# Kernel tuning notes

Hardware: AMD Instinct MI355X
Metric: run time of the kernel (lower is better)

## Reference

```python
import jax, jax.numpy as jnp
import numpy as np

T, B, IN, OUT, N_MOD, K = 1024, 8, 1024, 1024, 16, 2

def setup_inputs() -> dict:
    key = jax.random.key(0)
    k1, k2, k3, k4 = jax.random.split(key, 4)
    x = jax.random.normal(k1, (T, B, IN), dtype=jnp.float32)
    selection = jax.random.randint(k2, (B, K), 0, N_MOD, dtype=jnp.int64)
    weight = jax.random.normal(k3, (N_MOD, IN, OUT), dtype=jnp.float32) * (1.0 / np.sqrt(IN))
    bias = jax.random.normal(k4, (N_MOD, OUT), dtype=jnp.float32) * 0.02
    return {"x": x, "selection": selection, "weight": weight, "bias": bias}

def reference(x, selection, weight, bias):
    # time_major=True: x is [T, B, in] -> batch-major [B, T, in]
    xb = jnp.swapaxes(x, 0, 1)
    # Gather the K selected expert weight matrices per batch row: [B, K, in, out]
    W_sel = weight[selection]
    # Equivalent to matmul(x[i], cat(weight[sel], dim=1)): [B, T, K, out]
    o = jnp.einsum('bti,bkio->btko', xb, W_sel)
    Bn, Tn, Kn, On = o.shape
    o = o.reshape(Bn, Tn, Kn * On)
    # concat_dim == 1 bias: bias[sel].view(1, -1) -> [1, K*out], broadcast over T
    o = o + bias[selection].reshape(Bn, 1, Kn * On)
    # back to time-major [T, B, K*out]
    return jnp.swapaxes(o, 0, 1)
```

## Files before the change

kernel.cpp:

```cpp
#include <hip/hip_runtime.h>

#define T_DIM 1024
#define B_DIM 8
#define IN_DIM 1024
#define OUT_DIM 1024
#define N_MODL 16
#define K_SEL 2

typedef unsigned short ushort_t;
typedef __bf16 bf16x8 __attribute__((ext_vector_type(8)));
typedef float f32x4 __attribute__((ext_vector_type(4)));

__device__ __forceinline__ unsigned int f2bf2(float lo, float hi) {
  union { float f; unsigned int u; } a, b; a.f = lo; b.f = hi;
  unsigned int ra = (a.u + 0x7fffu + ((a.u >> 16) & 1u)) >> 16;
  unsigned int rb = (b.u + 0x7fffu + ((b.u >> 16) & 1u)) >> 16;
  return ra | (rb << 16);
}

__device__ __forceinline__ void async_g2l(const void* g, void* l) {
  __builtin_amdgcn_global_load_lds(
      (const __attribute__((address_space(1))) unsigned int*)g,
      (__attribute__((address_space(3))) unsigned int*)l,
      16, 0, 0);
}

__device__ __forceinline__ int read_sel(const int* __restrict__ s, int g) {
  bool i64 = true;
#pragma unroll
  for (int j = 0; j < 8; ++j) i64 &= (s[2 * j + 1] == 0);
  return i64 ? s[2 * g] : s[g];
}

__global__ __launch_bounds__(256) void convert_kernel(const float* __restrict__ x,
                                                      const float* __restrict__ w,
                                                      const int* __restrict__ selp,
                                                      ushort_t* __restrict__ xb,
                                                      ushort_t* __restrict__ wt) {
  __shared__ ushort_t tb[128 * 128];
  const int bid = blockIdx.x;
  if (bid >= 1024) {
    const int i = (bid - 1024) * 256 + threadIdx.x;
    const float4* s = (const float4*)x;
    float4 a = s[i * 2], b = s[i * 2 + 1];
    uint4 o;
    o.x = f2bf2(a.x, a.y); o.y = f2bf2(a.z, a.w);
    o.z = f2bf2(b.x, b.y); o.w = f2bf2(b.z, b.w);
    ((uint4*)xb)[i] = o;
    return;
  }
  const int m = bid >> 6;
  bool used = false;
#pragma unroll
  for (int g = 0; g < B_DIM * K_SEL; ++g) used |= (read_sel(selp, g) == m);
  if (!used) return;

  const int i0 = ((bid >> 3) & 7) * 128;
  const int o0 = (bid & 7) * 128;
  const float* src = w + ((size_t)(m * IN_DIM + i0)) * OUT_DIM + o0;

  const int o4 = (threadIdx.x & 31) * 4;
  const int ib = threadIdx.x >> 5;
#pragma unroll
  for (int p = 0; p < 16; ++p) {
    const int i = ib + p * 8;
    float4 v = *(const float4*)(src + (size_t)i * OUT_DIM + o4);
    const int osw = o4 ^ (((i >> 3) & 15) << 2);
    uint2 d2; d2.x = f2bf2(v.x, v.y); d2.y = f2bf2(v.z, v.w);
    *(uint2*)(tb + i * 128 + osw) = d2;
  }
  __syncthreads();

  ushort_t* dst = wt + ((size_t)(m * OUT_DIM + o0)) * IN_DIM + i0;
  const int il = (threadIdx.x & 15) * 8;
  const int ob = threadIdx.x >> 4;
  const int q2 = ((il >> 3) & 15) << 2;
#pragma unroll
  for (int p = 0; p < 8; ++p) {
    const int o = ob + p * 16;
    const int osw = o ^ q2;
    uint4 d;
    unsigned int u[8];
#pragma unroll
    for (int j = 0; j < 8; ++j) u[j] = tb[(il + j) * 128 + osw];
    d.x = u[0] | (u[1] << 16); d.y = u[2] | (u[3] << 16);
    d.z = u[4] | (u[5] << 16); d.w = u[6] | (u[7] << 16);
    *(uint4*)(dst + (size_t)o * IN_DIM + il) = d;
  }
}

#define MFMA16 __builtin_amdgcn_mfma_f32_16x16x32_bf16

template<bool LAST>
__device__ __forceinline__ void gstep(
    int t, ushort_t* As,
    const ushort_t* curB0, const ushort_t* curB1,
    ushort_t* nxtB0, ushort_t* nxtB1,
    const ushort_t* Ab, const ushort_t* Bb0, const ushort_t* Bb1,
    int wv, int ardo, int brdo, int cb,
    f32x4 (&acc0)[4][4], f32x4 (&acc1)[4][4]) {
  const int k1 = (t + 1) * 64;
  if (!LAST) {
#pragma unroll
    for (int c = 0; c < 4; ++c) {
      const int j = wv * 4 + c;
      async_g2l(Bb0 + (size_t)8 * j * IN_DIM + k1, nxtB0 + j * 512);
      async_g2l(Bb1 + (size_t)8 * j * IN_DIM + k1, nxtB1 + j * 512);
    }
    __builtin_amdgcn_sched_barrier(0);
  }
  bf16x8 af0[4], af1[4];
  const ushort_t* Ard = As + ardo;
#pragma unroll
  for (int i = 0; i < 4; ++i) {
    af0[i] = *(const bf16x8*)(Ard + i * 1024 + cb);
    af1[i] = *(const bf16x8*)(Ard + i * 1024 + (cb ^ 32));
  }
  if (!LAST) {
    __builtin_amdgcn_sched_barrier(0);
    asm volatile("s_waitcnt lgkmcnt(0)" ::: "memory");
    __builtin_amdgcn_sched_barrier(0);
    __builtin_amdgcn_s_barrier();
    __builtin_amdgcn_sched_barrier(0);
#pragma unroll
    for (int c = 0; c < 4; ++c) {
      const int j = wv * 4 + c;
      async_g2l(Ab + (size_t)8 * j * (B_DIM * IN_DIM) + k1, As + j * 512);
    }
    __builtin_amdgcn_sched_barrier(0);
  }
  const ushort_t* Brd0 = curB0 + brdo;
  const ushort_t* Brd1 = curB1 + brdo;
  bf16x8 b0[4], b1[4];
#pragma unroll
  for (int n = 0; n < 4; ++n) {
    b0[n] = *(const bf16x8*)(Brd0 + n * 1024 + cb);
    b1[n] = *(const bf16x8*)(Brd1 + n * 1024 + cb);
  }
  __builtin_amdgcn_s_setprio(1);
#pragma unroll
  for (int mt = 0; mt < 4; ++mt)
#pragma unroll
    for (int nt = 0; nt < 4; ++nt) {
      acc0[mt][nt] = MFMA16(af0[mt], b0[nt], acc0[mt][nt], 0, 0, 0);
      acc1[mt][nt] = MFMA16(af0[mt], b1[nt], acc1[mt][nt], 0, 0, 0);
    }
  __builtin_amdgcn_s_setprio(0);
#pragma unroll
  for (int n = 0; n < 4; ++n) {
    b0[n] = *(const bf16x8*)(Brd0 + n * 1024 + (cb ^ 32));
    b1[n] = *(const bf16x8*)(Brd1 + n * 1024 + (cb ^ 32));
  }
  __builtin_amdgcn_s_setprio(1);
#pragma unroll
  for (int mt = 0; mt < 4; ++mt)
#pragma unroll
    for (int nt = 0; nt < 4; ++nt) {
      acc0[mt][nt] = MFMA16(af1[mt], b0[nt], acc0[mt][nt], 0, 0, 0);
      acc1[mt][nt] = MFMA16(af1[mt], b1[nt], acc1[mt][nt], 0, 0, 0);
    }
  __builtin_amdgcn_s_setprio(0);
  if (!LAST) {
    __builtin_amdgcn_sched_barrier(0);
    asm volatile("s_waitcnt vmcnt(0)" ::: "memory");
    __builtin_amdgcn_sched_barrier(0);
    __builtin_amdgcn_s_barrier();
    __builtin_amdgcn_sched_barrier(0);
  }
}

__global__ __launch_bounds__(256, 2) void mlgemm_kernel(const ushort_t* __restrict__ xb,
                                                        const ushort_t* __restrict__ wt,
                                                        const int* __restrict__ selp,
                                                        const float* __restrict__ bias,
                                                        float* __restrict__ out) {
  __shared__ __align__(16) ushort_t smem[40960];
  ushort_t* As = smem;
#define BSP(buf, e) (smem + 8192 + ((buf) * 2 + (e)) * 8192)

  const int lin = blockIdx.x;
  const int b = lin & 7;
  const int mtile = (lin >> 3) & 7;
  const int ntile = lin >> 6;
  const int e0 = read_sel(selp, 2 * b);
  const int e1 = read_sel(selp, 2 * b + 1);
  const int m0 = mtile * 128;
  const int n0 = ntile * 128;

  const int tid = threadIdx.x;
  const int lane = tid & 63;
  const int wv = tid >> 6;

  const int srow = lane >> 3;
  const int sx = (((lane & 7) ^ (srow & 7)) << 3);
  const ushort_t* Ab  = xb + (size_t)(m0 + srow) * (B_DIM * IN_DIM) + b * IN_DIM + sx;
  const ushort_t* Bb0 = wt + ((size_t)(e0 * OUT_DIM + n0 + srow)) * IN_DIM + sx;
  const ushort_t* Bb1 = wt + ((size_t)(e1 * OUT_DIM + n0 + srow)) * IN_DIM + sx;

  const int frow = lane & 15;
  const int quad = lane >> 4;
  const int cb = ((quad ^ (frow & 7)) << 3);
  const int wrow = (wv & 1) * 64;
  const int wcol = (wv >> 1) * 64;
  const int ardo = (wrow + frow) * 64;
  const int brdo = (wcol + frow) * 64;

  f32x4 acc0[4][4] = {};
  f32x4 acc1[4][4] = {};

#pragma unroll
  for (int c = 0; c < 4; ++c) {
    const int j = wv * 4 + c;
    async_g2l(Ab  + (size_t)8 * j * (B_DIM * IN_DIM), As + j * 512);
    async_g2l(Bb0 + (size_t)8 * j * IN_DIM, BSP(0, 0) + j * 512);
    async_g2l(Bb1 + (size_t)8 * j * IN_DIM, BSP(0, 1) + j * 512);
  }
  __builtin_amdgcn_sched_barrier(0);
  asm volatile("s_waitcnt vmcnt(0)" ::: "memory");
  __builtin_amdgcn_sched_barrier(0);
  __builtin_amdgcn_s_barrier();
  __builtin_amdgcn_sched_barrier(0);

  for (int t = 0; t < 14; t += 2) {
    gstep<false>(t,     As, BSP(0, 0), BSP(0, 1), BSP(1, 0), BSP(1, 1),
                 Ab, Bb0, Bb1, wv, ardo, brdo, cb, acc0, acc1);
    gstep<false>(t + 1, As, BSP(1, 0), BSP(1, 1), BSP(0, 0), BSP(0, 1),
                 Ab, Bb0, Bb1, wv, ardo, brdo, cb, acc0, acc1);
  }
  gstep<false>(14, As, BSP(0, 0), BSP(0, 1), BSP(1, 0), BSP(1, 1),
               Ab, Bb0, Bb1, wv, ardo, brdo, cb, acc0, acc1);
  gstep<true>(15, As, BSP(1, 0), BSP(1, 1), BSP(0, 0), BSP(0, 1),
              Ab, Bb0, Bb1, wv, ardo, brdo, cb, acc0, acc1);

  __syncthreads();

  float* fb = (float*)smem;
  const float* bp0 = bias + (size_t)e0 * OUT_DIM;
  const float* bp1 = bias + (size_t)e1 * OUT_DIM;
  const int ocol0 = n0 + wcol + frow;
  float bv0[4], bv1[4];
#pragma unroll
  for (int nt = 0; nt < 4; ++nt) {
    bv0[nt] = bp0[ocol0 + nt * 16];
    bv1[nt] = bp1[ocol0 + nt * 16];
  }

#pragma unroll
  for (int r = 0; r < 2; ++r) {
    if ((wv & 1) == r) {
#pragma unroll
      for (int mt = 0; mt < 4; ++mt)
#pragma unroll
        for (int rr = 0; rr < 4; ++rr) {
          const int rowl = mt * 16 + quad * 4 + rr;
#pragma unroll
          for (int nt = 0; nt < 4; ++nt) {
            const int col = wcol + frow + nt * 16;
            fb[rowl * 260 + col]       = acc0[mt][nt][rr] + bv0[nt];
            fb[rowl * 260 + 128 + col] = acc1[mt][nt][rr] + bv1[nt];
          }
        }
    }
    __syncthreads();
    const int rl_base = tid >> 5;
    const int lir = tid & 31;
#pragma unroll
    for (int p = 0; p < 16; ++p) {
      const int e = p >> 3;
      const int rowl = (p & 7) * 8 + rl_base;
      const float* s = fb + rowl * 260 + e * 128 + lir * 4;
      float4 v = *(const float4*)s;
      const int grow = m0 + r * 64 + rowl;
      float* d = out + (size_t)grow * (B_DIM * K_SEL * OUT_DIM)
                     + (size_t)b * (K_SEL * OUT_DIM)
                     + (size_t)e * OUT_DIM + n0 + lir * 4;
      *(float4*)d = v;
    }
    __syncthreads();
  }
#undef BSP
}

extern "C" void kernel_launch(void* const* d_in, const int* in_sizes, int n_in,
                              void* d_out, int out_size, void* d_ws, size_t ws_size,
                              hipStream_t stream) {
  const float* x    = (const float*)d_in[0];
  const int*   sel  = (const int*)d_in[1];
  const float* w    = (const float*)d_in[2];
  const float* bias = (const float*)d_in[3];
  float* out = (float*)d_out;

  ushort_t* xb = (ushort_t*)d_ws;
  ushort_t* wt = (ushort_t*)((char*)d_ws +
                             (size_t)T_DIM * B_DIM * IN_DIM * 2);

  convert_kernel<<<dim3(1024 + T_DIM * B_DIM * IN_DIM / 8 / 256), 256, 0, stream>>>(
      x, w, sel, xb, wt);
  mlgemm_kernel<<<dim3(8 * 8 * B_DIM), 256, 0, stream>>>(xb, wt, sel, bias, out);
}
```

Before: 174.9 us.

## Fuse fp32-to-bf16 conversion of x into GEMM A-tile loading

Removes the separate pass that converts x to bf16 in a workspace. The GEMM now loads fp32 x directly into registers, converts to bf16 and writes the swizzled LDS tile itself. This saves a full write and re-read of the bf16 copy of x. In exchange, x is read in fp32 (twice the bytes) by each of the 8 n-tiles, and A loads become synchronous register loads instead of async LDS loads, which adds VGPR pressure and extra LDS store waits.

```diff
diff --git a/kernel.cpp b/kernel.cpp
--- a/kernel.cpp
+++ b/kernel.cpp
@@ -32,23 +32,11 @@
   return i64 ? s[2 * g] : s[g];
 }
 
-__global__ __launch_bounds__(256) void convert_kernel(const float* __restrict__ x,
-                                                      const float* __restrict__ w,
+__global__ __launch_bounds__(256) void convert_kernel(const float* __restrict__ w,
                                                       const int* __restrict__ selp,
-                                                      ushort_t* __restrict__ xb,
                                                       ushort_t* __restrict__ wt) {
   __shared__ ushort_t tb[128 * 128];
   const int bid = blockIdx.x;
-  if (bid >= 1024) {
-    const int i = (bid - 1024) * 256 + threadIdx.x;
-    const float4* s = (const float4*)x;
-    float4 a = s[i * 2], b = s[i * 2 + 1];
-    uint4 o;
-    o.x = f2bf2(a.x, a.y); o.y = f2bf2(a.z, a.w);
-    o.z = f2bf2(b.x, b.y); o.w = f2bf2(b.z, b.w);
-    ((uint4*)xb)[i] = o;
-    return;
-  }
   const int m = bid >> 6;
   bool used = false;
 #pragma unroll
@@ -96,11 +84,20 @@
     int t, ushort_t* As,
     const ushort_t* curB0, const ushort_t* curB1,
     ushort_t* nxtB0, ushort_t* nxtB1,
-    const ushort_t* Ab, const ushort_t* Bb0, const ushort_t* Bb1,
-    int wv, int ardo, int brdo, int cb,
+    const float* Af, const ushort_t* Bb0, const ushort_t* Bb1,
+    int wv, int ardo, int brdo, int cb, int awo,
     f32x4 (&acc0)[4][4], f32x4 (&acc1)[4][4]) {
   const int k1 = (t + 1) * 64;
+  float4 a4[4][2];
   if (!LAST) {
+#pragma unroll
+    for (int c = 0; c < 4; ++c) {
+      const int j = wv * 4 + c;
+      const float* ap = Af + (size_t)8 * j * (B_DIM * IN_DIM) + k1;
+      a4[c][0] = *(const float4*)(ap);
+      a4[c][1] = *(const float4*)(ap + 4);
+    }
+    __builtin_amdgcn_sched_barrier(0);
 #pragma unroll
     for (int c = 0; c < 4; ++c) {
       const int j = wv * 4 + c;
@@ -124,8 +121,10 @@
     __builtin_amdgcn_sched_barrier(0);
 #pragma unroll
     for (int c = 0; c < 4; ++c) {
-      const int j = wv * 4 + c;
-      async_g2l(Ab + (size_t)8 * j * (B_DIM * IN_DIM) + k1, As + j * 512);
+      uint4 o;
+      o.x = f2bf2(a4[c][0].x, a4[c][0].y); o.y = f2bf2(a4[c][0].z, a4[c][0].w);
+      o.z = f2bf2(a4[c][1].x, a4[c][1].y); o.w = f2bf2(a4[c][1].z, a4[c][1].w);
+      *(uint4*)(As + awo + c * 512) = o;
     }
     __builtin_amdgcn_sched_barrier(0);
   }
@@ -162,14 +161,14 @@
   __builtin_amdgcn_s_setprio(0);
   if (!LAST) {
     __builtin_amdgcn_sched_barrier(0);
-    asm volatile("s_waitcnt vmcnt(0)" ::: "memory");
+    asm volatile("s_waitcnt vmcnt(0) lgkmcnt(0)" ::: "memory");
     __builtin_amdgcn_sched_barrier(0);
     __builtin_amdgcn_s_barrier();
     __builtin_amdgcn_sched_barrier(0);
   }
 }
 
-__global__ __launch_bounds__(256, 2) void mlgemm_kernel(const ushort_t* __restrict__ xb,
+__global__ __launch_bounds__(256, 2) void mlgemm_kernel(const float* __restrict__ x,
                                                         const ushort_t* __restrict__ wt,
                                                         const int* __restrict__ selp,
                                                         const float* __restrict__ bias,
@@ -193,9 +192,10 @@
 
   const int srow = lane >> 3;
   const int sx = (((lane & 7) ^ (srow & 7)) << 3);
-  const ushort_t* Ab  = xb + (size_t)(m0 + srow) * (B_DIM * IN_DIM) + b * IN_DIM + sx;
+  const float*    Af  = x  + ((size_t)(m0 + srow) * B_DIM + b) * IN_DIM + sx;
   const ushort_t* Bb0 = wt + ((size_t)(e0 * OUT_DIM + n0 + srow)) * IN_DIM + sx;
   const ushort_t* Bb1 = wt + ((size_t)(e1 * OUT_DIM + n0 + srow)) * IN_DIM + sx;
+  const int awo = wv * 4 * 512 + lane * 8;
 
   const int frow = lane & 15;
   const int quad = lane >> 4;
@@ -208,29 +208,45 @@
   f32x4 acc0[4][4] = {};
   f32x4 acc1[4][4] = {};
 
-#pragma unroll
-  for (int c = 0; c < 4; ++c) {
-    const int j = wv * 4 + c;
-    async_g2l(Ab  + (size_t)8 * j * (B_DIM * IN_DIM), As + j * 512);
-    async_g2l(Bb0 + (size_t)8 * j * IN_DIM, BSP(0, 0) + j * 512);
-    async_g2l(Bb1 + (size_t)8 * j * IN_DIM, BSP(0, 1) + j * 512);
-  }
-  __builtin_amdgcn_sched_barrier(0);
-  asm volatile("s_waitcnt vmcnt(0)" ::: "memory");
-  __builtin_amdgcn_sched_barrier(0);
-  __builtin_amdgcn_s_barrier();
-  __builtin_amdgcn_sched_barrier(0);
+  {
+    float4 p4[4][2];
+#pragma unroll
+    for (int c = 0; c < 4; ++c) {
+      const int j = wv * 4 + c;
+      const float* ap = Af + (size_t)8 * j * (B_DIM * IN_DIM);
+      p4[c][0] = *(const float4*)(ap);
+      p4[c][1] = *(const float4*)(ap + 4);
+    }
+#pragma unroll
+    for (int c = 0; c < 4; ++c) {
+      const int j = wv * 4 + c;
+      async_g2l(Bb0 + (size_t)8 * j * IN_DIM, BSP(0, 0) + j * 512);
+      async_g2l(Bb1 + (size_t)8 * j * IN_DIM, BSP(0, 1) + j * 512);
+    }
+#pragma unroll
+    for (int c = 0; c < 4; ++c) {
+      uint4 o;
+      o.x = f2bf2(p4[c][0].x, p4[c][0].y); o.y = f2bf2(p4[c][0].z, p4[c][0].w);
+      o.z = f2bf2(p4[c][1].x, p4[c][1].y); o.w = f2bf2(p4[c][1].z, p4[c][1].w);
+      *(uint4*)(As + awo + c * 512) = o;
+    }
+    __builtin_amdgcn_sched_barrier(0);
+    asm volatile("s_waitcnt vmcnt(0) lgkmcnt(0)" ::: "memory");
+    __builtin_amdgcn_sched_barrier(0);
+    __builtin_amdgcn_s_barrier();
+    __builtin_amdgcn_sched_barrier(0);
+  }
 
   for (int t = 0; t < 14; t += 2) {
     gstep<false>(t,     As, BSP(0, 0), BSP(0, 1), BSP(1, 0), BSP(1, 1),
-                 Ab, Bb0, Bb1, wv, ardo, brdo, cb, acc0, acc1);
+                 Af, Bb0, Bb1, wv, ardo, brdo, cb, awo, acc0, acc1);
     gstep<false>(t + 1, As, BSP(1, 0), BSP(1, 1), BSP(0, 0), BSP(0, 1),
-                 Ab, Bb0, Bb1, wv, ardo, brdo, cb, acc0, acc1);
+                 Af, Bb0, Bb1, wv, ardo, brdo, cb, awo, acc0, acc1);
   }
   gstep<false>(14, As, BSP(0, 0), BSP(0, 1), BSP(1, 0), BSP(1, 1),
-               Ab, Bb0, Bb1, wv, ardo, brdo, cb, acc0, acc1);
+               Af, Bb0, Bb1, wv, ardo, brdo, cb, awo, acc0, acc1);
   gstep<true>(15, As, BSP(1, 0), BSP(1, 1), BSP(0, 0), BSP(0, 1),
-              Ab, Bb0, Bb1, wv, ardo, brdo, cb, acc0, acc1);
+              Af, Bb0, Bb1, wv, ardo, brdo, cb, awo, acc0, acc1);
 
   __syncthreads();
 
@@ -290,11 +306,8 @@
   const float* bias = (const float*)d_in[3];
   float* out = (float*)d_out;
 
-  ushort_t* xb = (ushort_t*)d_ws;
-  ushort_t* wt = (ushort_t*)((char*)d_ws +
-                             (size_t)T_DIM * B_DIM * IN_DIM * 2);
-
-  convert_kernel<<<dim3(1024 + T_DIM * B_DIM * IN_DIM / 8 / 256), 256, 0, stream>>>(
-      x, w, sel, xb, wt);
-  mlgemm_kernel<<<dim3(8 * 8 * B_DIM), 256, 0, stream>>>(xb, wt, sel, bias, out);
-}
+  ushort_t* wt = (ushort_t*)d_ws;
+
+  convert_kernel<<<dim3(1024), 256, 0, stream>>>(w, sel, wt);
+  mlgemm_kernel<<<dim3(8 * 8 * B_DIM), 256, 0, stream>>>(x, wt, sel, bias, out);
+}
```

New measurement: 223.0 us. 1.27x slower.
